# Kernel optimization log

Hardware: AMD Instinct MI355X
Metric: run time of the kernel (lower is better)

## Reference

```python
import jax, jax.numpy as jnp
import numpy as np

N_NODES = 50000
N_GRAPHS = 64
D = 320


def gcn_conv(x, W, b, src, dst, n):
    # PyG GCNConv (default): add self loops, symmetric deg^-1/2 normalization,
    # linear transform, scatter-add aggregation at target, plus bias.
    h = x @ W  # [N, d_out]
    loop = jnp.arange(n)
    s = jnp.concatenate([src, loop])
    t = jnp.concatenate([dst, loop])
    deg = jax.ops.segment_sum(jnp.ones_like(t, dtype=h.dtype), t, num_segments=n)
    dinv = jnp.where(deg > 0, jax.lax.rsqrt(deg), 0.0)
    norm = dinv[s] * dinv[t]  # [E+N]
    msg = h[s] * norm[:, None]  # gather + scale, [E+N, d_out]
    out = jax.ops.segment_sum(msg, t, num_segments=n)
    return out + b


def setup_inputs() -> dict:
    key = jax.random.key(0)
    ks = jax.random.split(key, 12)
    x = jax.random.normal(ks[0], (N_NODES, D), dtype=jnp.float32)
    edge_index = jax.random.randint(ks[1], (2, 800000), 0, N_NODES, dtype=jnp.int64)
    batch = jnp.sort(jax.random.randint(ks[2], (N_NODES,), 0, N_GRAPHS, dtype=jnp.int64))

    def lin(k, fan_in, fan_out):
        bound = 1.0 / np.sqrt(fan_in)
        kw, kb = jax.random.split(k)
        W = jax.random.uniform(kw, (fan_in, fan_out), minval=-bound, maxval=bound, dtype=jnp.float32)
        b = jax.random.uniform(kb, (fan_out,), minval=-bound, maxval=bound, dtype=jnp.float32)
        return W, b

    W1, b1 = lin(ks[3], D, D)
    W2, b2 = lin(ks[4], D, D)
    W3, b3 = lin(ks[5], D, D)
    Wf1, bf1 = lin(ks[6], D, 256)
    Wf2, bf2 = lin(ks[7], 256, 16)
    Wf3, bf3 = lin(ks[8], 16, 1)
    return {"x": x, "W1": W1, "b1": b1, "W2": W2, "b2": b2, "W3": W3, "b3": b3,
            "Wf1": Wf1, "bf1": bf1, "Wf2": Wf2, "bf2": bf2, "Wf3": Wf3, "bf3": bf3,
            "edge_index": edge_index, "batch": batch}


def reference(x, W1, b1, W2, b2, W3, b3, Wf1, bf1, Wf2, bf2, Wf3, bf3, edge_index, batch):
    src, dst = edge_index[0], edge_index[1]
    n = x.shape[0]
    h = jax.nn.relu(gcn_conv(x, W1, b1, src, dst, n))
    h = jax.nn.relu(gcn_conv(h, W2, b2, src, dst, n))
    h = jax.nn.relu(gcn_conv(h, W3, b3, src, dst, n))
    g = jax.ops.segment_max(h, batch, num_segments=N_GRAPHS)  # global max pool [B, D]
    g = jax.nn.relu(g @ Wf1 + bf1)  # dropout is identity in eval mode
    g = jax.nn.relu(g @ Wf2 + bf2)
    return g @ Wf3 + bf3
```

## Files before the change

### kernel.cpp

```cpp
#include <hip/hip_runtime.h>
#include <hip/hip_bf16.h>

#define N_NODES 50000
#define N_EDGES 800000
#define N_GRAPHS 64
#define D 320
#define CAP 64
#define POOL_SPLIT 4

typedef __attribute__((ext_vector_type(8))) short s16x8;
typedef __attribute__((ext_vector_type(4))) float f32x4;
typedef __attribute__((ext_vector_type(4))) unsigned int u32x4;

__device__ inline ushort f2bf(float f) {
    __hip_bfloat16 h = __float2bfloat16(f);
    return *reinterpret_cast<ushort*>(&h);
}

__global__ __launch_bounds__(256) void k_prep(const float* __restrict__ W1,
                                              const float* __restrict__ W2,
                                              const float* __restrict__ W3,
                                              ushort* __restrict__ Wt,
                                              int* __restrict__ cursor) {
    int i = blockIdx.x * blockDim.x + threadIdx.x;
    if (i < N_NODES) cursor[i] = 0;
    if (i < 3 * D * D) {
        int w = i / (D * D), r = i % (D * D);
        const float* W = (w == 0) ? W1 : (w == 1) ? W2 : W3;
        int k = r / D, n = r % D;
        Wt[w * D * D + n * D + k] = f2bf(W[r]);
    }
}

__global__ void k_fill(const int* __restrict__ src, const int* __restrict__ dst,
                       int* __restrict__ cursor, int* __restrict__ csr) {
    int e = blockIdx.x * blockDim.x + threadIdx.x;
    if (e < N_EDGES) {
        int d = dst[e];
        int p = atomicAdd(&cursor[d], 1);
        if (p < CAP) csr[d * CAP + p] = src[e];
    }
}

#define GBM 128
#define GBK 32
#define LDK 40
template<int AMODE>
__global__ __launch_bounds__(512) void k_gemm(const void* __restrict__ Ain,
                                              const ushort* __restrict__ Wt,
                                              const int* __restrict__ cursor,
                                              ushort* __restrict__ P) {
    __shared__ ushort As[GBM][LDK];
    __shared__ ushort Bs[D][LDK];
    int t = threadIdx.x;
    int m0 = blockIdx.x * GBM;
    int lane = t & 63;
    int wid = t >> 6;
    int wm = wid & 1;
    int wn = wid >> 1;
    int r16 = lane & 15;
    int kb = (lane >> 4) * 8;

    f32x4 acc[4][5] = {};

    for (int k0 = 0; k0 < D; k0 += GBK) {
        #pragma unroll
        for (int u = 0; u < 4; ++u) {
            int gi = t + 512 * u;
            if (gi < 512) {
                int r = gi >> 2, s = gi & 3;
                int gr = m0 + r;
                s16x8 v = {};
                if (gr < N_NODES) {
                    int k = k0 + s * 8;
                    if constexpr (AMODE == 1) {
                        const float* Af = (const float*)Ain;
                        float4 a0 = *(const float4*)&Af[(size_t)gr * D + k];
                        float4 a1 = *(const float4*)&Af[(size_t)gr * D + k + 4];
                        v[0] = (short)f2bf(a0.x); v[1] = (short)f2bf(a0.y);
                        v[2] = (short)f2bf(a0.z); v[3] = (short)f2bf(a0.w);
                        v[4] = (short)f2bf(a1.x); v[5] = (short)f2bf(a1.y);
                        v[6] = (short)f2bf(a1.z); v[7] = (short)f2bf(a1.w);
                    } else {
                        const ushort* Ab = (const ushort*)Ain;
                        v = *(const s16x8*)&Ab[(size_t)gr * D + k];
                    }
                }
                *(s16x8*)&As[r][s * 8] = v;
            } else if (gi < 1792) {
                int gj = gi - 512;
                int r = gj >> 2, s = gj & 3;
                *(s16x8*)&Bs[r][s * 8] = *(const s16x8*)&Wt[(size_t)r * D + k0 + s * 8];
            }
        }
        __syncthreads();

        s16x8 af[4], bfr[5];
        #pragma unroll
        for (int mi = 0; mi < 4; ++mi)
            af[mi] = *(const s16x8*)&As[wm * 64 + mi * 16 + r16][kb];
        #pragma unroll
        for (int ni = 0; ni < 5; ++ni)
            bfr[ni] = *(const s16x8*)&Bs[wn * 80 + ni * 16 + r16][kb];
        #pragma unroll
        for (int mi = 0; mi < 4; ++mi)
            #pragma unroll
            for (int ni = 0; ni < 5; ++ni)
                acc[mi][ni] = __builtin_amdgcn_mfma_f32_16x16x32_bf16(af[mi], bfr[ni], acc[mi][ni], 0, 0, 0);
        __syncthreads();
    }

    #pragma unroll
    for (int mi = 0; mi < 4; ++mi) {
        int rbase = m0 + wm * 64 + mi * 16 + (lane >> 4) * 4;
        #pragma unroll
        for (int r = 0; r < 4; ++r) {
            int row = rbase + r;
            if (row < N_NODES) {
                float dv = rsqrtf((float)(cursor[row] + 1));
                #pragma unroll
                for (int ni = 0; ni < 5; ++ni) {
                    int col = wn * 80 + ni * 16 + r16;
                    P[(size_t)row * D + col] = f2bf(acc[mi][ni][r] * dv);
                }
            }
        }
    }
}

#define AGG_NPB 8
__global__ __launch_bounds__(320) void k_agg(const ushort* __restrict__ P,
                                             const int* __restrict__ cursor,
                                             const int* __restrict__ csr,
                                             const float* __restrict__ bias,
                                             ushort* __restrict__ H) {
    int t = threadIdx.x;
    int nl = t / 40;
    int cg = t - nl * 40;
    int n  = blockIdx.x * AGG_NPB + nl;
    int c0 = cg * 8;
    size_t row = (size_t)n * D + c0;
    const char* Pb = (const char*)P;
    unsigned coff = (unsigned)(c0 * 2);

    f32x4 aE = {}, aO = {};
    {
        u32x4 u = *(const u32x4*)&P[row];
        aE += __builtin_bit_cast(f32x4, u << 16);
        aO += __builtin_bit_cast(f32x4, u & (unsigned int)0xffff0000u);
    }
    int cnt = cursor[n];
    int deg = cnt > CAP ? CAP : cnt;
    const int* lst = csr + n * CAP;
    int i = 0;
    for (; i + 4 <= deg; i += 4) {
        int s0 = lst[i], s1 = lst[i + 1], s2 = lst[i + 2], s3 = lst[i + 3];
        u32x4 u0 = *(const u32x4*)(Pb + (unsigned)s0 * (unsigned)(D * 2) + coff);
        u32x4 u1 = *(const u32x4*)(Pb + (unsigned)s1 * (unsigned)(D * 2) + coff);
        u32x4 u2 = *(const u32x4*)(Pb + (unsigned)s2 * (unsigned)(D * 2) + coff);
        u32x4 u3 = *(const u32x4*)(Pb + (unsigned)s3 * (unsigned)(D * 2) + coff);
        aE += __builtin_bit_cast(f32x4, u0 << 16);
        aO += __builtin_bit_cast(f32x4, u0 & (unsigned int)0xffff0000u);
        aE += __builtin_bit_cast(f32x4, u1 << 16);
        aO += __builtin_bit_cast(f32x4, u1 & (unsigned int)0xffff0000u);
        aE += __builtin_bit_cast(f32x4, u2 << 16);
        aO += __builtin_bit_cast(f32x4, u2 & (unsigned int)0xffff0000u);
        aE += __builtin_bit_cast(f32x4, u3 << 16);
        aO += __builtin_bit_cast(f32x4, u3 & (unsigned int)0xffff0000u);
    }
    for (; i < deg; ++i) {
        int s = lst[i];
        u32x4 u = *(const u32x4*)(Pb + (unsigned)s * (unsigned)(D * 2) + coff);
        aE += __builtin_bit_cast(f32x4, u << 16);
        aO += __builtin_bit_cast(f32x4, u & (unsigned int)0xffff0000u);
    }
    float dv = rsqrtf((float)(cnt + 1));
    s16x8 ov;
    #pragma unroll
    for (int q = 0; q < 4; ++q) {
        float e = fmaxf(fmaf(dv, aE[q], bias[c0 + 2 * q]), 0.0f);
        float o = fmaxf(fmaf(dv, aO[q], bias[c0 + 2 * q + 1]), 0.0f);
        ov[2 * q]     = (short)f2bf(e);
        ov[2 * q + 1] = (short)f2bf(o);
    }
    *(s16x8*)&H[row] = ov;
}

__global__ __launch_bounds__(320) void k_pool(const ushort* __restrict__ H,
                                              const int* __restrict__ batch,
                                              float* __restrict__ Gp) {
    __shared__ int range[2];
    int sp = blockIdx.x;
    int b = blockIdx.y;
    int t = threadIdx.x;
    int nl = t / 40;
    int cg = t - nl * 40;
    int c0 = cg * 8;
    if (t < 2) {
        int target = b + t;
        int lo = 0, hi = N_NODES;
        while (lo < hi) {
            int mid = (lo + hi) >> 1;
            if (batch[mid] < target) lo = mid + 1; else hi = mid;
        }
        range[t] = lo;
    }
    __syncthreads();
    int s = range[0], e = range[1];
    f32x4 mE = {}, mO = {};
    for (int n = s + sp * 8 + nl; n < e; n += POOL_SPLIT * 8) {
        u32x4 u = *(const u32x4*)&H[(size_t)n * D + c0];
        f32x4 vE = __builtin_bit_cast(f32x4, u << 16);
        f32x4 vO = __builtin_bit_cast(f32x4, u & (unsigned int)0xffff0000u);
        #pragma unroll
        for (int q = 0; q < 4; ++q) {
            mE[q] = fmaxf(mE[q], vE[q]);
            mO[q] = fmaxf(mO[q], vO[q]);
        }
    }
    __shared__ float red[8][D];
    #pragma unroll
    for (int q = 0; q < 4; ++q) {
        red[nl][c0 + 2 * q]     = mE[q];
        red[nl][c0 + 2 * q + 1] = mO[q];
    }
    __syncthreads();
    if (nl == 0) {
        #pragma unroll
        for (int q = 0; q < 8; ++q) {
            int c = c0 + q;
            float m = red[0][c];
            #pragma unroll
            for (int r = 1; r < 8; ++r) m = fmaxf(m, red[r][c]);
            Gp[(sp * N_GRAPHS + b) * D + c] = m;
        }
    }
}

__global__ __launch_bounds__(256) void k_mlp(const float* __restrict__ Gp,
    const float* __restrict__ Wf1, const float* __restrict__ bf1,
    const float* __restrict__ Wf2, const float* __restrict__ bf2,
    const float* __restrict__ Wf3, const float* __restrict__ bf3,
    float* __restrict__ out) {
    __shared__ float g_s[D];
    __shared__ float s1[256];
    __shared__ float s2[16];
    int b = blockIdx.x;
    int t = threadIdx.x;
    for (int i = t; i < D; i += 256) {
        float m = Gp[b * D + i];
        #pragma unroll
        for (int sp = 1; sp < POOL_SPLIT; ++sp)
            m = fmaxf(m, Gp[(sp * N_GRAPHS + b) * D + i]);
        g_s[i] = m;
    }
    __syncthreads();
    float acc = bf1[t];
    for (int k = 0; k < D; ++k) acc = fmaf(g_s[k], Wf1[k * 256 + t], acc);
    s1[t] = fmaxf(acc, 0.0f);
    __syncthreads();
    if (t < 16) {
        float a2 = bf2[t];
        for (int k = 0; k < 256; ++k) a2 = fmaf(s1[k], Wf2[k * 16 + t], a2);
        s2[t] = fmaxf(a2, 0.0f);
    }
    __syncthreads();
    if (t == 0) {
        float a3 = bf3[0];
        #pragma unroll
        for (int k = 0; k < 16; ++k) a3 = fmaf(s2[k], Wf3[k], a3);
        out[b] = a3;
    }
}

extern "C" void kernel_launch(void* const* d_in, const int* in_sizes, int n_in,
                              void* d_out, int out_size, void* d_ws, size_t ws_size,
                              hipStream_t stream) {
    const float* x   = (const float*)d_in[0];
    const float* W1  = (const float*)d_in[1];
    const float* b1  = (const float*)d_in[2];
    const float* W2  = (const float*)d_in[3];
    const float* b2  = (const float*)d_in[4];
    const float* W3  = (const float*)d_in[5];
    const float* b3  = (const float*)d_in[6];
    const float* Wf1 = (const float*)d_in[7];
    const float* bf1 = (const float*)d_in[8];
    const float* Wf2 = (const float*)d_in[9];
    const float* bf2 = (const float*)d_in[10];
    const float* Wf3 = (const float*)d_in[11];
    const float* bf3 = (const float*)d_in[12];
    const int*   ei  = (const int*)d_in[13];
    const int*   src = ei;
    const int*   dst = ei + N_EDGES;
    const int*   batch = (const int*)d_in[14];
    float* out = (float*)d_out;

    char* p = (char*)d_ws;
    auto alloc = [&](size_t bytes) { char* r = p; p += (bytes + 255) & ~(size_t)255; return (void*)r; };
    const size_t NB = (size_t)N_NODES * D * sizeof(ushort);
    ushort* bB   = (ushort*)alloc(NB);
    ushort* bC   = (ushort*)alloc(NB);
    ushort* Wt   = (ushort*)alloc(3 * D * D * 2);
    int*    cursor = (int*)alloc(N_NODES * 4);
    int*    csr  = (int*)alloc((size_t)N_NODES * CAP * 4);
    float*  Gp   = (float*)alloc(POOL_SPLIT * N_GRAPHS * D * 4);

    k_prep<<<(3 * D * D + 255) / 256, 256, 0, stream>>>(W1, W2, W3, Wt, cursor);
    k_fill<<<(N_EDGES + 255) / 256, 256, 0, stream>>>(src, dst, cursor, csr);

    int ggrid = (N_NODES + GBM - 1) / GBM;
    int agrid = N_NODES / AGG_NPB;
    k_gemm<1><<<ggrid, 512, 0, stream>>>(x, Wt, cursor, bB);
    k_agg<<<agrid, 320, 0, stream>>>(bB, cursor, csr, b1, bC);
    k_gemm<0><<<ggrid, 512, 0, stream>>>(bC, Wt + D * D, cursor, bB);
    k_agg<<<agrid, 320, 0, stream>>>(bB, cursor, csr, b2, bC);
    k_gemm<0><<<ggrid, 512, 0, stream>>>(bC, Wt + 2 * D * D, cursor, bB);
    k_agg<<<agrid, 320, 0, stream>>>(bB, cursor, csr, b3, bC);
    dim3 pgrid(POOL_SPLIT, N_GRAPHS);
    k_pool<<<pgrid, 320, 0, stream>>>(bC, batch, Gp);
    k_mlp<<<N_GRAPHS, 256, 0, stream>>>(Gp, Wf1, bf1, Wf2, bf2, Wf3, bf3, out);
}
```

Baseline: 381.6 us.

## Halve GEMM row tile and prefetch next K-slice into registers

```diff
diff --git a/kernel.cpp b/kernel.cpp
--- a/kernel.cpp
+++ b/kernel.cpp
@@ -42,9 +42,10 @@
     }
 }
 
-#define GBM 128
+#define GBM 64
 #define GBK 32
 #define LDK 40
+#define KSTEPS (D / GBK)
 template<int AMODE>
 __global__ __launch_bounds__(512) void k_gemm(const void* __restrict__ Ain,
                                               const ushort* __restrict__ Wt,
@@ -61,49 +62,74 @@
     int r16 = lane & 15;
     int kb = (lane >> 4) * 8;
 
-    f32x4 acc[4][5] = {};
-
-    for (int k0 = 0; k0 < D; k0 += GBK) {
-        #pragma unroll
-        for (int u = 0; u < 4; ++u) {
-            int gi = t + 512 * u;
-            if (gi < 512) {
-                int r = gi >> 2, s = gi & 3;
-                int gr = m0 + r;
-                s16x8 v = {};
-                if (gr < N_NODES) {
-                    int k = k0 + s * 8;
-                    if constexpr (AMODE == 1) {
-                        const float* Af = (const float*)Ain;
-                        float4 a0 = *(const float4*)&Af[(size_t)gr * D + k];
-                        float4 a1 = *(const float4*)&Af[(size_t)gr * D + k + 4];
-                        v[0] = (short)f2bf(a0.x); v[1] = (short)f2bf(a0.y);
-                        v[2] = (short)f2bf(a0.z); v[3] = (short)f2bf(a0.w);
-                        v[4] = (short)f2bf(a1.x); v[5] = (short)f2bf(a1.y);
-                        v[6] = (short)f2bf(a1.z); v[7] = (short)f2bf(a1.w);
-                    } else {
-                        const ushort* Ab = (const ushort*)Ain;
-                        v = *(const s16x8*)&Ab[(size_t)gr * D + k];
-                    }
-                }
-                *(s16x8*)&As[r][s * 8] = v;
-            } else if (gi < 1792) {
-                int gj = gi - 512;
-                int r = gj >> 2, s = gj & 3;
-                *(s16x8*)&Bs[r][s * 8] = *(const s16x8*)&Wt[(size_t)r * D + k0 + s * 8];
+    int ar = t >> 2, as = t & 3;
+    int agr = m0 + ar;
+    bool aok = (t < 256) && (agr < N_NODES);
+
+    f32x4 acc[2][5] = {};
+    s16x8 aReg;
+    s16x8 bReg0, bReg1, bReg2;
+    bool b2ok = (t + 1024) < 1280;
+
+    auto loadA = [&](int k0) {
+        s16x8 v = {};
+        if (aok) {
+            int k = k0 + as * 8;
+            if constexpr (AMODE == 1) {
+                const float* Af = (const float*)Ain;
+                float4 a0 = *(const float4*)&Af[(size_t)agr * D + k];
+                float4 a1 = *(const float4*)&Af[(size_t)agr * D + k + 4];
+                v[0] = (short)f2bf(a0.x); v[1] = (short)f2bf(a0.y);
+                v[2] = (short)f2bf(a0.z); v[3] = (short)f2bf(a0.w);
+                v[4] = (short)f2bf(a1.x); v[5] = (short)f2bf(a1.y);
+                v[6] = (short)f2bf(a1.z); v[7] = (short)f2bf(a1.w);
+            } else {
+                const ushort* Ab = (const ushort*)Ain;
+                v = *(const s16x8*)&Ab[(size_t)agr * D + k];
             }
         }
+        aReg = v;
+    };
+    auto loadB = [&](int k0) {
+        bReg0 = *(const s16x8*)&Wt[(size_t)(t >> 2) * D + k0 + (t & 3) * 8];
+        int g1 = t + 512;
+        bReg1 = *(const s16x8*)&Wt[(size_t)(g1 >> 2) * D + k0 + (g1 & 3) * 8];
+        if (b2ok) {
+            int g2 = t + 1024;
+            bReg2 = *(const s16x8*)&Wt[(size_t)(g2 >> 2) * D + k0 + (g2 & 3) * 8];
+        }
+    };
+
+    loadA(0);
+    loadB(0);
+
+    for (int kk = 0; kk < KSTEPS; ++kk) {
+        if (t < 256) *(s16x8*)&As[ar][as * 8] = aReg;
+        *(s16x8*)&Bs[t >> 2][(t & 3) * 8] = bReg0;
+        {
+            int g1 = t + 512;
+            *(s16x8*)&Bs[g1 >> 2][(g1 & 3) * 8] = bReg1;
+            if (b2ok) {
+                int g2 = t + 1024;
+                *(s16x8*)&Bs[g2 >> 2][(g2 & 3) * 8] = bReg2;
+            }
+        }
         __syncthreads();
 
-        s16x8 af[4], bfr[5];
-        #pragma unroll
-        for (int mi = 0; mi < 4; ++mi)
-            af[mi] = *(const s16x8*)&As[wm * 64 + mi * 16 + r16][kb];
+        if (kk + 1 < KSTEPS) {
+            loadA((kk + 1) * GBK);
+            loadB((kk + 1) * GBK);
+        }
+
+        s16x8 af[2], bfr[5];
+        #pragma unroll
+        for (int mi = 0; mi < 2; ++mi)
+            af[mi] = *(const s16x8*)&As[wm * 32 + mi * 16 + r16][kb];
         #pragma unroll
         for (int ni = 0; ni < 5; ++ni)
             bfr[ni] = *(const s16x8*)&Bs[wn * 80 + ni * 16 + r16][kb];
         #pragma unroll
-        for (int mi = 0; mi < 4; ++mi)
+        for (int mi = 0; mi < 2; ++mi)
             #pragma unroll
             for (int ni = 0; ni < 5; ++ni)
                 acc[mi][ni] = __builtin_amdgcn_mfma_f32_16x16x32_bf16(af[mi], bfr[ni], acc[mi][ni], 0, 0, 0);
@@ -111,8 +137,8 @@
     }
 
     #pragma unroll
-    for (int mi = 0; mi < 4; ++mi) {
-        int rbase = m0 + wm * 64 + mi * 16 + (lane >> 4) * 4;
+    for (int mi = 0; mi < 2; ++mi) {
+        int rbase = m0 + wm * 32 + mi * 16 + (lane >> 4) * 4;
         #pragma unroll
         for (int r = 0; r < 4; ++r) {
             int row = rbase + r;
```

New measurement: 391.6 us. 1.03x slower.
